# Performance work log

Hardware: AMD Instinct MI355X
Metric: run time of the kernel (lower is better)

The kernel has to match this reference:

```python
import jax, jax.numpy as jnp
import numpy as np

B, N, DIM_S, E = 128, 2048, 128, 128


def _xavier(key, shape):
    fan_out, fan_in = shape[0], shape[1]
    limit = float(np.sqrt(6.0 / (fan_in + fan_out)))
    return jax.random.uniform(key, shape, jnp.float32, -limit, limit)


def setup_inputs() -> dict:
    key = jax.random.key(0)
    ks = jax.random.split(key, 14)
    return {
        "instance": jax.random.normal(ks[0], (B, N, DIM_S), jnp.float32),
        # conv1d kernel-size-1 embeds == per-node linear layers [out, in]
        "W_s": _xavier(ks[1], (E, DIM_S)),
        "b_s": jnp.zeros((E,), jnp.float32),
        "W_a": _xavier(ks[2], (E, E)),
        "b_a": jnp.zeros((E,), jnp.float32),
        "v_a": jax.random.normal(ks[3], (E,), jnp.float32),
        "W_c": _xavier(ks[4], (E, 2 * E)),
        "b_c": jnp.zeros((E,), jnp.float32),
        "v_c": jax.random.normal(ks[5], (E,), jnp.float32),
        "W1": _xavier(ks[6], (E, E)),
        "b1": jnp.zeros((E,), jnp.float32),
        "W2": _xavier(ks[7], (1, E)),
        "b2": jnp.zeros((1,), jnp.float32),
    }


def reference(instance, W_s, b_s, W_a, b_a, v_a, W_c, b_c, v_c, W1, b1, W2, b2):
    # project_s: conv1d k=1 == linear over feature dim. [B,N,E]
    proj = jnp.einsum("bns,es->bne", instance, W_s) + b_s
    # first additive-attention score: v_a . tanh(w_a(proj))  -> [B,N]
    u_t = jnp.einsum("bne,e->bn", jnp.tanh(jnp.einsum("bne,fe->bnf", proj, W_a) + b_a), v_a)
    a_t = jax.nn.softmax(u_t, axis=1)  # softmax over nodes
    c_t = a_t[:, :, None] * proj  # [B,N,E]
    hidden_2 = jnp.concatenate([proj, c_t], axis=2)  # [B,N,2E]
    u_t_2 = jnp.einsum("bne,e->bn", jnp.tanh(jnp.einsum("bnf,ef->bne", hidden_2, W_c) + b_c), v_c)
    prob = jax.nn.softmax(u_t_2, axis=1)  # [B,N]
    h_i = jnp.einsum("bn,bne->be", prob, proj)  # weighted sum -> [B,E]
    out1 = jax.nn.relu(h_i @ W1.T + b1)  # [B,E]
    v = (out1 @ W2.T + b2)[:, 0]  # [B]
    return v
```

## Files before the change

### kernel.cpp

```cpp
#include <hip/hip_runtime.h>
#include <hip/hip_bf16.h>

typedef _Float16 half8 __attribute__((ext_vector_type(8)));
typedef _Float16 half4v __attribute__((ext_vector_type(4)));
typedef float f32x4 __attribute__((ext_vector_type(4)));

#define SWZ(byte, r) ((unsigned)(byte) ^ ((((unsigned)(r)) & 7u) << 4))

constexpr int Bb = 128;
constexpr int Nn = 2048;
constexpr int Ee = 128;
constexpr int BM1 = 128;
constexpr int P1_BLOCKS = 256;
constexpr int P1_ITERS = (Bb * Nn) / BM1 / P1_BLOCKS;

constexpr size_t OFF_W    = 0;
constexpr size_t OFF_PROJ = 131072;
constexpr size_t OFF_UT   = OFF_PROJ + (size_t)Bb * Nn * Ee * 2;
constexpr size_t OFF_UT2  = OFF_UT   + (size_t)Bb * Nn * 4;
constexpr size_t OFF_HP   = OFF_UT2  + (size_t)Bb * Nn * 4;

__device__ __forceinline__ void cp16(void* lds, const void* g) {
    __builtin_amdgcn_global_load_lds(
        (const __attribute__((address_space(1))) unsigned int*)g,
        (__attribute__((address_space(3))) unsigned int*)lds, 16, 0, 0);
}

__device__ __forceinline__ float fast_tanh(float x) {
    float e = __expf(2.0f * x);
    return 1.0f - 2.0f * __builtin_amdgcn_rcpf(e + 1.0f);
}

__global__ __launch_bounds__(256) void k_prep(const float* __restrict__ Ws,
                                              const float* __restrict__ Wa,
                                              const float* __restrict__ Wc,
                                              char* __restrict__ wdst)
{
    int id = blockIdx.x * 256 + threadIdx.x;
    for (int i = id; i < 65536; i += 64 * 256) {
        int mat = i >> 14;
        int rem = i & 16383;
        int r = rem >> 7, c = rem & 127;
        float v;
        if      (mat == 0) v = Ws[r * 128 + c];
        else if (mat == 1) v = Wa[r * 128 + c];
        else if (mat == 2) v = Wc[r * 256 + c];
        else               v = Wc[r * 256 + 128 + c];
        unsigned off = SWZ((unsigned)((r * 128 + c) * 2), r);
        *reinterpret_cast<_Float16*>(wdst + (size_t)mat * 32768 + off) = (_Float16)v;
    }
}

__global__ __launch_bounds__(512) void k_pass1(const float* __restrict__ inst,
                                               const char* __restrict__ wtiles,
                                               const float* __restrict__ bs,
                                               const float* __restrict__ ba,
                                               const float* __restrict__ va,
                                               char* __restrict__ projg,
                                               float* __restrict__ ut)
{
    __shared__ _Float16 ldsW[2 * 16384];
    __shared__ _Float16 bufA[2][16384];

    const int tid  = threadIdx.x;
    const int lane = tid & 63;
    const int w    = tid >> 6;
    const int l15  = lane & 15;
    const int kg   = lane >> 4;
    const int arow = w * 16 + l15;

    #pragma unroll
    for (int i = 0; i < 8; ++i) {
        unsigned o = (unsigned)((i * 512 + tid) * 16);
        cp16((char*)ldsW + o, wtiles + o);
    }

    const size_t tile0 = (size_t)blockIdx.x * P1_ITERS;
    float4 v[8];
    {
        const float* src = inst + tile0 * BM1 * 128;
        #pragma unroll
        for (int i = 0; i < 8; ++i)
            v[i] = *reinterpret_cast<const float4*>(src + (size_t)(i * 512 + tid) * 4);
    }
    #pragma unroll
    for (int i = 0; i < 8; ++i) {
        int f = i * 512 + tid;
        int r = f >> 5, c4 = f & 31;
        half4v h = { (_Float16)v[i].x, (_Float16)v[i].y, (_Float16)v[i].z, (_Float16)v[i].w };
        *reinterpret_cast<half4v*>((char*)bufA[0] + SWZ(r * 256 + c4 * 8, r)) = h;
    }
    __syncthreads();

    for (int it = 0; it < P1_ITERS; ++it) {
        const int cur = it & 1, nxt = cur ^ 1;
        const size_t row0 = (tile0 + it) * BM1;

        if (it + 1 < P1_ITERS) {
            const float* src = inst + (row0 + BM1) * 128;
            #pragma unroll
            for (int i = 0; i < 8; ++i)
                v[i] = *reinterpret_cast<const float4*>(src + (size_t)(i * 512 + tid) * 4);
        }

        f32x4 acc[8];
        #pragma unroll
        for (int fr = 0; fr < 8; ++fr) acc[fr] = f32x4{0.f, 0.f, 0.f, 0.f};
        #pragma unroll
        for (int kk = 0; kk < 4; ++kk) {
            half8 af = *reinterpret_cast<const half8*>(
                (char*)bufA[cur] + SWZ(arow * 256 + kk * 64 + kg * 16, arow));
            #pragma unroll
            for (int fr = 0; fr < 8; ++fr) {
                int br = fr * 16 + l15;
                half8 bf = *reinterpret_cast<const half8*>(
                    (char*)ldsW + SWZ(br * 256 + kk * 64 + kg * 16, br));
                acc[fr] = __builtin_amdgcn_mfma_f32_16x16x32_f16(af, bf, acc[fr], 0, 0, 0);
            }
        }
        __syncthreads();

        #pragma unroll
        for (int fr = 0; fr < 8; ++fr) {
            int e = fr * 16 + l15;
            float bsv = bs[e];
            #pragma unroll
            for (int j = 0; j < 4; ++j) {
                int r = w * 16 + kg * 4 + j;
                *reinterpret_cast<_Float16*>((char*)bufA[cur] + SWZ(r * 256 + e * 2, r)) =
                    (_Float16)(acc[fr][j] + bsv);
            }
        }
        if (it + 1 < P1_ITERS) {
            #pragma unroll
            for (int i = 0; i < 8; ++i) {
                int f = i * 512 + tid;
                int r = f >> 5, c4 = f & 31;
                half4v h = { (_Float16)v[i].x, (_Float16)v[i].y, (_Float16)v[i].z, (_Float16)v[i].w };
                *reinterpret_cast<half4v*>((char*)bufA[nxt] + SWZ(r * 256 + c4 * 8, r)) = h;
            }
        }
        __syncthreads();

        f32x4 tac[8];
        #pragma unroll
        for (int fr = 0; fr < 8; ++fr) tac[fr] = f32x4{0.f, 0.f, 0.f, 0.f};
        #pragma unroll
        for (int kk = 0; kk < 4; ++kk) {
            half8 af = *reinterpret_cast<const half8*>(
                (char*)bufA[cur] + SWZ(arow * 256 + kk * 64 + kg * 16, arow));
            #pragma unroll
            for (int fr = 0; fr < 8; ++fr) {
                int br = fr * 16 + l15;
                half8 bf = *reinterpret_cast<const half8*>(
                    (char*)ldsW + 32768 + SWZ(br * 256 + kk * 64 + kg * 16, br));
                tac[fr] = __builtin_amdgcn_mfma_f32_16x16x32_f16(af, bf, tac[fr], 0, 0, 0);
            }
        }

        {
            char* dst = projg + row0 * 256;
            #pragma unroll
            for (int i = 0; i < 4; ++i) {
                unsigned o = (unsigned)((i * 512 + tid) * 16);
                *reinterpret_cast<uint4*>(dst + o) =
                    *reinterpret_cast<const uint4*>((const char*)bufA[cur] + o);
            }
        }

        float u[4] = {0.f, 0.f, 0.f, 0.f};
        #pragma unroll
        for (int fr = 0; fr < 8; ++fr) {
            int fcol = fr * 16 + l15;
            float vav = va[fcol], bav = ba[fcol];
            #pragma unroll
            for (int j = 0; j < 4; ++j)
                u[j] += vav * fast_tanh(tac[fr][j] + bav);
        }
        #pragma unroll
        for (int d = 1; d < 16; d <<= 1) {
            #pragma unroll
            for (int j = 0; j < 4; ++j) u[j] += __shfl_xor(u[j], d);
        }
        if (l15 == 0) {
            #pragma unroll
            for (int j = 0; j < 4; ++j)
                ut[row0 + w * 16 + kg * 4 + j] = u[j];
        }
    }
}

__global__ __launch_bounds__(512) void k_pass2(const char* __restrict__ projg,
                                               const char* __restrict__ wtiles,
                                               const float* __restrict__ bc,
                                               const float* __restrict__ vc,
                                               const float* __restrict__ ut,
                                               float* __restrict__ ut2)
{
    __shared__ _Float16 ldsW[2 * 16384];
    __shared__ _Float16 bufP[2][16384];
    __shared__ float at_lds[1024];
    __shared__ float redm[8], reds[8];

    const int tid  = threadIdx.x;
    const int lane = tid & 63;
    const int w    = tid >> 6;
    const int l15  = lane & 15;
    const int kg   = lane >> 4;
    const int arow = w * 16 + l15;
    const int bid  = blockIdx.x;
    const int batch = bid >> 1, half = bid & 1;

    const float* utb = ut + (size_t)batch * Nn;
    float4 x = *reinterpret_cast<const float4*>(utb + tid * 4);
    float m = fmaxf(fmaxf(x.x, x.y), fmaxf(x.z, x.w));
    #pragma unroll
    for (int d = 1; d < 64; d <<= 1) m = fmaxf(m, __shfl_xor(m, d));
    if (lane == 0) redm[w] = m;
    __syncthreads();
    float M = redm[0];
    #pragma unroll
    for (int k = 1; k < 8; ++k) M = fmaxf(M, redm[k]);
    float e0 = __expf(x.x - M), e1 = __expf(x.y - M), e2 = __expf(x.z - M), e3 = __expf(x.w - M);
    float s = e0 + e1 + e2 + e3;
    #pragma unroll
    for (int d = 1; d < 64; d <<= 1) s += __shfl_xor(s, d);
    if (lane == 0) reds[w] = s;
    __syncthreads();
    float S = 0.f;
    #pragma unroll
    for (int k = 0; k < 8; ++k) S += reds[k];
    float invS = 1.0f / S;

    #pragma unroll
    for (int i = 0; i < 8; ++i) {
        unsigned o = (unsigned)((i * 512 + tid) * 16);
        cp16((char*)ldsW + o, wtiles + 65536 + o);
    }
    const char* psrc = projg + ((size_t)batch * Nn + (size_t)half * 1024) * 256;
    #pragma unroll
    for (int i = 0; i < 4; ++i) {
        unsigned o = (unsigned)((i * 512 + tid) * 16);
        cp16((char*)bufP[0] + o, psrc + o);
    }
    if ((tid >> 8) == half) {
        int rl = (tid & 255) * 4;
        at_lds[rl + 0] = e0 * invS;
        at_lds[rl + 1] = e1 * invS;
        at_lds[rl + 2] = e2 * invS;
        at_lds[rl + 3] = e3 * invS;
    }

    for (int it = 0; it < 8; ++it) {
        const int cur = it & 1, nxt = cur ^ 1;
        __syncthreads();

        if (it + 1 < 8) {
            #pragma unroll
            for (int i = 0; i < 4; ++i) {
                unsigned o = (unsigned)((i * 512 + tid) * 16);
                cp16((char*)bufP[nxt] + o, psrc + (size_t)(it + 1) * 32768 + o);
            }
        }

        f32x4 u1[8], u2[8];
        #pragma unroll
        for (int fr = 0; fr < 8; ++fr) { u1[fr] = f32x4{0.f,0.f,0.f,0.f}; u2[fr] = f32x4{0.f,0.f,0.f,0.f}; }
        #pragma unroll
        for (int kk = 0; kk < 4; ++kk) {
            half8 af = *reinterpret_cast<const half8*>(
                (char*)bufP[cur] + SWZ(arow * 256 + kk * 64 + kg * 16, arow));
            #pragma unroll
            for (int fr = 0; fr < 8; ++fr) {
                int br = fr * 16 + l15;
                half8 bf1 = *reinterpret_cast<const half8*>(
                    (char*)ldsW + SWZ(br * 256 + kk * 64 + kg * 16, br));
                u1[fr] = __builtin_amdgcn_mfma_f32_16x16x32_f16(af, bf1, u1[fr], 0, 0, 0);
                half8 bf2 = *reinterpret_cast<const half8*>(
                    (char*)ldsW + 32768 + SWZ(br * 256 + kk * 64 + kg * 16, br));
                u2[fr] = __builtin_amdgcn_mfma_f32_16x16x32_f16(af, bf2, u2[fr], 0, 0, 0);
            }
        }

        float aj[4];
        #pragma unroll
        for (int j = 0; j < 4; ++j) aj[j] = at_lds[it * 128 + w * 16 + kg * 4 + j];
        float u[4] = {0.f, 0.f, 0.f, 0.f};
        #pragma unroll
        for (int fr = 0; fr < 8; ++fr) {
            int fcol = fr * 16 + l15;
            float vcv = vc[fcol], bcv = bc[fcol];
            #pragma unroll
            for (int j = 0; j < 4; ++j)
                u[j] += vcv * fast_tanh(u1[fr][j] + aj[j] * u2[fr][j] + bcv);
        }
        #pragma unroll
        for (int d = 1; d < 16; d <<= 1) {
            #pragma unroll
            for (int j = 0; j < 4; ++j) u[j] += __shfl_xor(u[j], d);
        }
        if (l15 == 0) {
            #pragma unroll
            for (int j = 0; j < 4; ++j)
                ut2[(size_t)batch * Nn + (size_t)half * 1024 + it * 128 + w * 16 + kg * 4 + j] = u[j];
        }
    }
}

__global__ __launch_bounds__(256) void k_hi(const float* __restrict__ ut2,
                                            const char* __restrict__ projg,
                                            float* __restrict__ hpart)
{
    __shared__ float pw[128];
    __shared__ float hp[16][128];
    __shared__ float redm[4], reds[4];

    const int bid = blockIdx.x;
    const int b = bid >> 4, chunk = bid & 15;
    const int n0 = chunk * 128;
    const int tid = threadIdx.x;
    const int lane = tid & 63, w = tid >> 6;

    const float* u2b = ut2 + (size_t)b * Nn;
    float4 x0 = *reinterpret_cast<const float4*>(u2b + tid * 8);
    float4 x1 = *reinterpret_cast<const float4*>(u2b + tid * 8 + 4);
    float m = fmaxf(fmaxf(fmaxf(x0.x, x0.y), fmaxf(x0.z, x0.w)),
                    fmaxf(fmaxf(x1.x, x1.y), fmaxf(x1.z, x1.w)));
    #pragma unroll
    for (int d = 1; d < 64; d <<= 1) m = fmaxf(m, __shfl_xor(m, d));
    if (lane == 0) redm[w] = m;
    __syncthreads();
    float M = fmaxf(fmaxf(redm[0], redm[1]), fmaxf(redm[2], redm[3]));
    float e[8] = { __expf(x0.x - M), __expf(x0.y - M), __expf(x0.z - M), __expf(x0.w - M),
                   __expf(x1.x - M), __expf(x1.y - M), __expf(x1.z - M), __expf(x1.w - M) };
    float s = 0.f;
    #pragma unroll
    for (int i = 0; i < 8; ++i) s += e[i];
    #pragma unroll
    for (int d = 1; d < 64; d <<= 1) s += __shfl_xor(s, d);
    if (lane == 0) reds[w] = s;
    __syncthreads();
    float inv = 1.0f / (reds[0] + reds[1] + reds[2] + reds[3]);
    if ((tid >> 4) == chunk) {
        int base = (tid & 15) * 8;
        #pragma unroll
        for (int k = 0; k < 8; ++k) pw[base + k] = e[k] * inv;
    }
    __syncthreads();

    const int rg = tid >> 4, c16 = tid & 15;
    const char* pb = projg + ((size_t)b * Nn + n0) * 256;
    float acc[8] = {0.f,0.f,0.f,0.f,0.f,0.f,0.f,0.f};
    #pragma unroll
    for (int itn = 0; itn < 8; ++itn) {
        int nl = rg + itn * 16;
        float wgt = pw[nl];
        unsigned off = (unsigned)(nl * 256 + ((c16 * 16) ^ ((nl & 7) << 4)));
        half8 ph = *reinterpret_cast<const half8*>(pb + off);
        #pragma unroll
        for (int j = 0; j < 8; ++j) acc[j] += wgt * (float)ph[j];
    }
    #pragma unroll
    for (int j = 0; j < 8; ++j) hp[rg][c16 * 8 + j] = acc[j];
    __syncthreads();
    if (tid < 128) {
        float s2 = 0.f;
        #pragma unroll
        for (int k = 0; k < 16; ++k) s2 += hp[k][tid];
        hpart[((size_t)b * 16 + chunk) * 128 + tid] = s2;
    }
}

__global__ __launch_bounds__(128) void k_head(const float* __restrict__ hpart,
                                              const float* __restrict__ W1,
                                              const float* __restrict__ b1,
                                              const float* __restrict__ W2,
                                              const float* __restrict__ b2,
                                              float* __restrict__ out)
{
    __shared__ float h[128];
    __shared__ float o1[128];
    const int b = blockIdx.x, tid = threadIdx.x;

    float s = 0.f;
    #pragma unroll
    for (int c = 0; c < 16; ++c) s += hpart[((size_t)b * 16 + c) * 128 + tid];
    h[tid] = s;
    __syncthreads();

    const float* wr = W1 + tid * 128;
    float o = b1[tid];
    #pragma unroll 8
    for (int e = 0; e < 128; e += 4) {
        float4 wv = *reinterpret_cast<const float4*>(wr + e);
        o += wv.x * h[e] + wv.y * h[e+1] + wv.z * h[e+2] + wv.w * h[e+3];
    }
    o1[tid] = fmaxf(o, 0.f);
    __syncthreads();

    if (tid < 64) {
        float p = o1[tid] * W2[tid] + o1[tid + 64] * W2[tid + 64];
        #pragma unroll
        for (int d = 1; d < 64; d <<= 1) p += __shfl_xor(p, d);
        if (tid == 0) out[b] = p + b2[0];
    }
}

extern "C" void kernel_launch(void* const* d_in, const int* in_sizes, int n_in,
                              void* d_out, int out_size, void* d_ws, size_t ws_size,
                              hipStream_t stream)
{
    const float* inst = (const float*)d_in[0];
    const float* Ws   = (const float*)d_in[1];
    const float* bs   = (const float*)d_in[2];
    const float* Wa   = (const float*)d_in[3];
    const float* ba   = (const float*)d_in[4];
    const float* va   = (const float*)d_in[5];
    const float* Wc   = (const float*)d_in[6];
    const float* bc   = (const float*)d_in[7];
    const float* vc   = (const float*)d_in[8];
    const float* W1   = (const float*)d_in[9];
    const float* b1   = (const float*)d_in[10];
    const float* W2   = (const float*)d_in[11];
    const float* b2   = (const float*)d_in[12];
    float* out = (float*)d_out;

    char*  ws     = (char*)d_ws;
    char*  wtiles = ws + OFF_W;
    char*  projg  = ws + OFF_PROJ;
    float* ut     = (float*)(ws + OFF_UT);
    float* ut2    = (float*)(ws + OFF_UT2);
    float* hpart  = (float*)(ws + OFF_HP);

    hipLaunchKernelGGL(k_prep,  dim3(64),        dim3(256), 0, stream, Ws, Wa, Wc, wtiles);
    hipLaunchKernelGGL(k_pass1, dim3(P1_BLOCKS), dim3(512), 0, stream, inst, wtiles, bs, ba, va, projg, ut);
    hipLaunchKernelGGL(k_pass2, dim3(Bb * 2),    dim3(512), 0, stream, projg, wtiles, bc, vc, ut, ut2);
    hipLaunchKernelGGL(k_hi,    dim3(Bb * 16),   dim3(256), 0, stream, ut2, projg, hpart);
    hipLaunchKernelGGL(k_head,  dim3(Bb),        dim3(128), 0, stream, hpart, W1, b1, W2, b2, out);
}
```

Before: 285.1 us.

## Halve block size and tile rows in both attention passes to cut LDS

k_pass1 and k_pass2 now use 256-thread blocks working on 64-row tiles with a single LDS activation buffer instead of 512 threads, 128 rows and double buffering. The grids double to 512 blocks, and LDS per block drops so more blocks can be resident per CU, aiming to improve latency hiding. Pass2 now prefetches the next proj tile through registers instead of async global-to-LDS copies. It also reuses the buffer as scratch for the softmax reductions and attention weights. The trade-off is extra barriers and less intra-block overlap, since one buffer is written and read each iteration.

```diff
diff --git a/kernel.cpp b/kernel.cpp
--- a/kernel.cpp
+++ b/kernel.cpp
@@ -10,9 +10,6 @@
 constexpr int Bb = 128;
 constexpr int Nn = 2048;
 constexpr int Ee = 128;
-constexpr int BM1 = 128;
-constexpr int P1_BLOCKS = 256;
-constexpr int P1_ITERS = (Bb * Nn) / BM1 / P1_BLOCKS;
 
 constexpr size_t OFF_W    = 0;
 constexpr size_t OFF_PROJ = 131072;
@@ -51,7 +48,7 @@
     }
 }
 
-__global__ __launch_bounds__(512) void k_pass1(const float* __restrict__ inst,
+__global__ __launch_bounds__(256) void k_pass1(const float* __restrict__ inst,
                                                const char* __restrict__ wtiles,
                                                const float* __restrict__ bs,
                                                const float* __restrict__ ba,
@@ -60,7 +57,7 @@
                                                float* __restrict__ ut)
 {
     __shared__ _Float16 ldsW[2 * 16384];
-    __shared__ _Float16 bufA[2][16384];
+    __shared__ _Float16 buf[8192];
 
     const int tid  = threadIdx.x;
     const int lane = tid & 63;
@@ -70,37 +67,37 @@
     const int arow = w * 16 + l15;
 
     #pragma unroll
-    for (int i = 0; i < 8; ++i) {
-        unsigned o = (unsigned)((i * 512 + tid) * 16);
+    for (int i = 0; i < 16; ++i) {
+        unsigned o = (unsigned)((i * 256 + tid) * 16);
         cp16((char*)ldsW + o, wtiles + o);
     }
 
-    const size_t tile0 = (size_t)blockIdx.x * P1_ITERS;
+    const size_t tile0 = (size_t)blockIdx.x * 8;
     float4 v[8];
     {
-        const float* src = inst + tile0 * BM1 * 128;
+        const float* src = inst + tile0 * 64 * 128;
         #pragma unroll
         for (int i = 0; i < 8; ++i)
-            v[i] = *reinterpret_cast<const float4*>(src + (size_t)(i * 512 + tid) * 4);
-    }
-    #pragma unroll
-    for (int i = 0; i < 8; ++i) {
-        int f = i * 512 + tid;
-        int r = f >> 5, c4 = f & 31;
-        half4v h = { (_Float16)v[i].x, (_Float16)v[i].y, (_Float16)v[i].z, (_Float16)v[i].w };
-        *reinterpret_cast<half4v*>((char*)bufA[0] + SWZ(r * 256 + c4 * 8, r)) = h;
-    }
-    __syncthreads();
-
-    for (int it = 0; it < P1_ITERS; ++it) {
-        const int cur = it & 1, nxt = cur ^ 1;
-        const size_t row0 = (tile0 + it) * BM1;
-
-        if (it + 1 < P1_ITERS) {
-            const float* src = inst + (row0 + BM1) * 128;
+            v[i] = *reinterpret_cast<const float4*>(src + (size_t)(i * 256 + tid) * 4);
+    }
+
+    for (int it = 0; it < 8; ++it) {
+        const size_t row0 = (tile0 + it) * 64;
+
+        #pragma unroll
+        for (int i = 0; i < 8; ++i) {
+            int f = i * 256 + tid;
+            int r = f >> 5, c4 = f & 31;
+            half4v h = { (_Float16)v[i].x, (_Float16)v[i].y, (_Float16)v[i].z, (_Float16)v[i].w };
+            *reinterpret_cast<half4v*>((char*)buf + SWZ(r * 256 + c4 * 8, r)) = h;
+        }
+        __syncthreads();
+
+        if (it + 1 < 8) {
+            const float* src = inst + (row0 + 64) * 128;
             #pragma unroll
             for (int i = 0; i < 8; ++i)
-                v[i] = *reinterpret_cast<const float4*>(src + (size_t)(i * 512 + tid) * 4);
+                v[i] = *reinterpret_cast<const float4*>(src + (size_t)(i * 256 + tid) * 4);
         }
 
         f32x4 acc[8];
@@ -109,7 +106,7 @@
         #pragma unroll
         for (int kk = 0; kk < 4; ++kk) {
             half8 af = *reinterpret_cast<const half8*>(
-                (char*)bufA[cur] + SWZ(arow * 256 + kk * 64 + kg * 16, arow));
+                (char*)buf + SWZ(arow * 256 + kk * 64 + kg * 16, arow));
             #pragma unroll
             for (int fr = 0; fr < 8; ++fr) {
                 int br = fr * 16 + l15;
@@ -127,19 +124,10 @@
             #pragma unroll
             for (int j = 0; j < 4; ++j) {
                 int r = w * 16 + kg * 4 + j;
-                *reinterpret_cast<_Float16*>((char*)bufA[cur] + SWZ(r * 256 + e * 2, r)) =
+                *reinterpret_cast<_Float16*>((char*)buf + SWZ(r * 256 + e * 2, r)) =
                     (_Float16)(acc[fr][j] + bsv);
             }
         }
-        if (it + 1 < P1_ITERS) {
-            #pragma unroll
-            for (int i = 0; i < 8; ++i) {
-                int f = i * 512 + tid;
-                int r = f >> 5, c4 = f & 31;
-                half4v h = { (_Float16)v[i].x, (_Float16)v[i].y, (_Float16)v[i].z, (_Float16)v[i].w };
-                *reinterpret_cast<half4v*>((char*)bufA[nxt] + SWZ(r * 256 + c4 * 8, r)) = h;
-            }
-        }
         __syncthreads();
 
         f32x4 tac[8];
@@ -148,7 +136,7 @@
         #pragma unroll
         for (int kk = 0; kk < 4; ++kk) {
             half8 af = *reinterpret_cast<const half8*>(
-                (char*)bufA[cur] + SWZ(arow * 256 + kk * 64 + kg * 16, arow));
+                (char*)buf + SWZ(arow * 256 + kk * 64 + kg * 16, arow));
             #pragma unroll
             for (int fr = 0; fr < 8; ++fr) {
                 int br = fr * 16 + l15;
@@ -162,9 +150,9 @@
             char* dst = projg + row0 * 256;
             #pragma unroll
             for (int i = 0; i < 4; ++i) {
-                unsigned o = (unsigned)((i * 512 + tid) * 16);
+                unsigned o = (unsigned)((i * 256 + tid) * 16);
                 *reinterpret_cast<uint4*>(dst + o) =
-                    *reinterpret_cast<const uint4*>((const char*)bufA[cur] + o);
+                    *reinterpret_cast<const uint4*>((const char*)buf + o);
             }
         }
 
@@ -187,10 +175,11 @@
             for (int j = 0; j < 4; ++j)
                 ut[row0 + w * 16 + kg * 4 + j] = u[j];
         }
-    }
-}
-
-__global__ __launch_bounds__(512) void k_pass2(const char* __restrict__ projg,
+        __syncthreads();
+    }
+}
+
+__global__ __launch_bounds__(256) void k_pass2(const char* __restrict__ projg,
                                                const char* __restrict__ wtiles,
                                                const float* __restrict__ bc,
                                                const float* __restrict__ vc,
@@ -198,9 +187,8 @@
                                                float* __restrict__ ut2)
 {
     __shared__ _Float16 ldsW[2 * 16384];
-    __shared__ _Float16 bufP[2][16384];
-    __shared__ float at_lds[1024];
-    __shared__ float redm[8], reds[8];
+    __shared__ _Float16 buf[8192];
+    float* scratch = reinterpret_cast<float*>(buf);
 
     const int tid  = threadIdx.x;
     const int lane = tid & 63;
@@ -209,58 +197,67 @@
     const int kg   = lane >> 4;
     const int arow = w * 16 + l15;
     const int bid  = blockIdx.x;
-    const int batch = bid >> 1, half = bid & 1;
+    const int batch = bid >> 2, quarter = bid & 3;
+
+    #pragma unroll
+    for (int i = 0; i < 16; ++i) {
+        unsigned o = (unsigned)((i * 256 + tid) * 16);
+        cp16((char*)ldsW + o, wtiles + 65536 + o);
+    }
 
     const float* utb = ut + (size_t)batch * Nn;
-    float4 x = *reinterpret_cast<const float4*>(utb + tid * 4);
-    float m = fmaxf(fmaxf(x.x, x.y), fmaxf(x.z, x.w));
+    float4 x0 = *reinterpret_cast<const float4*>(utb + tid * 8);
+    float4 x1 = *reinterpret_cast<const float4*>(utb + tid * 8 + 4);
+    float m = fmaxf(fmaxf(fmaxf(x0.x, x0.y), fmaxf(x0.z, x0.w)),
+                    fmaxf(fmaxf(x1.x, x1.y), fmaxf(x1.z, x1.w)));
     #pragma unroll
     for (int d = 1; d < 64; d <<= 1) m = fmaxf(m, __shfl_xor(m, d));
-    if (lane == 0) redm[w] = m;
-    __syncthreads();
-    float M = redm[0];
-    #pragma unroll
-    for (int k = 1; k < 8; ++k) M = fmaxf(M, redm[k]);
-    float e0 = __expf(x.x - M), e1 = __expf(x.y - M), e2 = __expf(x.z - M), e3 = __expf(x.w - M);
-    float s = e0 + e1 + e2 + e3;
+    if (lane == 0) scratch[w] = m;
+    __syncthreads();
+    float M = fmaxf(fmaxf(scratch[0], scratch[1]), fmaxf(scratch[2], scratch[3]));
+    float e[8] = { __expf(x0.x - M), __expf(x0.y - M), __expf(x0.z - M), __expf(x0.w - M),
+                   __expf(x1.x - M), __expf(x1.y - M), __expf(x1.z - M), __expf(x1.w - M) };
+    float s = 0.f;
+    #pragma unroll
+    for (int i = 0; i < 8; ++i) s += e[i];
     #pragma unroll
     for (int d = 1; d < 64; d <<= 1) s += __shfl_xor(s, d);
-    if (lane == 0) reds[w] = s;
-    __syncthreads();
-    float S = 0.f;
-    #pragma unroll
-    for (int k = 0; k < 8; ++k) S += reds[k];
-    float invS = 1.0f / S;
-
-    #pragma unroll
-    for (int i = 0; i < 8; ++i) {
-        unsigned o = (unsigned)((i * 512 + tid) * 16);
-        cp16((char*)ldsW + o, wtiles + 65536 + o);
-    }
-    const char* psrc = projg + ((size_t)batch * Nn + (size_t)half * 1024) * 256;
+    __syncthreads();
+    if (lane == 0) scratch[4 + w] = s;
+    __syncthreads();
+    float invS = 1.0f / (scratch[4] + scratch[5] + scratch[6] + scratch[7]);
+    if ((tid >> 6) == quarter * 4 / 4 && tid >= quarter * 64 && tid < quarter * 64 + 64) {
+        int base = tid * 8 - quarter * 512;
+        #pragma unroll
+        for (int k = 0; k < 8; ++k) scratch[8 + base + k] = e[k] * invS;
+    }
+    __syncthreads();
+    float aj[8][4];
+    #pragma unroll
+    for (int t = 0; t < 8; ++t) {
+        #pragma unroll
+        for (int j = 0; j < 4; ++j)
+            aj[t][j] = scratch[8 + t * 64 + w * 16 + kg * 4 + j];
+    }
+    __syncthreads();
+
+    const char* psrc = projg + ((size_t)batch * Nn + (size_t)quarter * 512) * 256;
     #pragma unroll
     for (int i = 0; i < 4; ++i) {
-        unsigned o = (unsigned)((i * 512 + tid) * 16);
-        cp16((char*)bufP[0] + o, psrc + o);
-    }
-    if ((tid >> 8) == half) {
-        int rl = (tid & 255) * 4;
-        at_lds[rl + 0] = e0 * invS;
-        at_lds[rl + 1] = e1 * invS;
-        at_lds[rl + 2] = e2 * invS;
-        at_lds[rl + 3] = e3 * invS;
-    }
-
-    for (int it = 0; it < 8; ++it) {
-        const int cur = it & 1, nxt = cur ^ 1;
-        __syncthreads();
-
-        if (it + 1 < 8) {
-            #pragma unroll
-            for (int i = 0; i < 4; ++i) {
-                unsigned o = (unsigned)((i * 512 + tid) * 16);
-                cp16((char*)bufP[nxt] + o, psrc + (size_t)(it + 1) * 32768 + o);
-            }
+        unsigned o = (unsigned)((i * 256 + tid) * 16);
+        cp16((char*)buf + o, psrc + o);
+    }
+
+    uint4 pv[4];
+    #pragma unroll
+    for (int t = 0; t < 8; ++t) {
+        __syncthreads();
+
+        if (t + 1 < 8) {
+            const char* nsrc = psrc + (size_t)(t + 1) * 16384;
+            #pragma unroll
+            for (int i = 0; i < 4; ++i)
+                pv[i] = *reinterpret_cast<const uint4*>(nsrc + (i * 256 + tid) * 16);
         }
 
         f32x4 u1[8], u2[8];
@@ -269,7 +266,7 @@
         #pragma unroll
         for (int kk = 0; kk < 4; ++kk) {
             half8 af = *reinterpret_cast<const half8*>(
-                (char*)bufP[cur] + SWZ(arow * 256 + kk * 64 + kg * 16, arow));
+                (char*)buf + SWZ(arow * 256 + kk * 64 + kg * 16, arow));
             #pragma unroll
             for (int fr = 0; fr < 8; ++fr) {
                 int br = fr * 16 + l15;
@@ -282,9 +279,6 @@
             }
         }
 
-        float aj[4];
-        #pragma unroll
-        for (int j = 0; j < 4; ++j) aj[j] = at_lds[it * 128 + w * 16 + kg * 4 + j];
         float u[4] = {0.f, 0.f, 0.f, 0.f};
         #pragma unroll
         for (int fr = 0; fr < 8; ++fr) {
@@ -292,7 +286,7 @@
             float vcv = vc[fcol], bcv = bc[fcol];
             #pragma unroll
             for (int j = 0; j < 4; ++j)
-                u[j] += vcv * fast_tanh(u1[fr][j] + aj[j] * u2[fr][j] + bcv);
+                u[j] += vcv * fast_tanh(u1[fr][j] + aj[t][j] * u2[fr][j] + bcv);
         }
         #pragma unroll
         for (int d = 1; d < 16; d <<= 1) {
@@ -302,7 +296,13 @@
         if (l15 == 0) {
             #pragma unroll
             for (int j = 0; j < 4; ++j)
-                ut2[(size_t)batch * Nn + (size_t)half * 1024 + it * 128 + w * 16 + kg * 4 + j] = u[j];
+                ut2[(size_t)batch * Nn + (size_t)quarter * 512 + t * 64 + w * 16 + kg * 4 + j] = u[j];
+        }
+        __syncthreads();
+        if (t + 1 < 8) {
+            #pragma unroll
+            for (int i = 0; i < 4; ++i)
+                *reinterpret_cast<uint4*>((char*)buf + (i * 256 + tid) * 16) = pv[i];
         }
     }
 }
@@ -432,9 +432,9 @@
     float* ut2    = (float*)(ws + OFF_UT2);
     float* hpart  = (float*)(ws + OFF_HP);
 
-    hipLaunchKernelGGL(k_prep,  dim3(64),        dim3(256), 0, stream, Ws, Wa, Wc, wtiles);
-    hipLaunchKernelGGL(k_pass1, dim3(P1_BLOCKS), dim3(512), 0, stream, inst, wtiles, bs, ba, va, projg, ut);
-    hipLaunchKernelGGL(k_pass2, dim3(Bb * 2),    dim3(512), 0, stream, projg, wtiles, bc, vc, ut, ut2);
-    hipLaunchKernelGGL(k_hi,    dim3(Bb * 16),   dim3(256), 0, stream, ut2, projg, hpart);
-    hipLaunchKernelGGL(k_head,  dim3(Bb),        dim3(128), 0, stream, hpart, W1, b1, W2, b2, out);
-}
+    hipLaunchKernelGGL(k_prep,  dim3(64),      dim3(256), 0, stream, Ws, Wa, Wc, wtiles);
+    hipLaunchKernelGGL(k_pass1, dim3(512),     dim3(256), 0, stream, inst, wtiles, bs, ba, va, projg, ut);
+    hipLaunchKernelGGL(k_pass2, dim3(512),     dim3(256), 0, stream, projg, wtiles, bc, vc, ut, ut2);
+    hipLaunchKernelGGL(k_hi,    dim3(Bb * 16), dim3(256), 0, stream, ut2, projg, hpart);
+    hipLaunchKernelGGL(k_head,  dim3(Bb),      dim3(128), 0, stream, hpart, W1, b1, W2, b2, out);
+}
```

Result: slower. 297.1 us (+4.2%).
